# Kernel optimization log

Hardware: AMD Instinct MI355X
Metric: run time of the kernel (lower is better)

Reference implementation:

```python
import jax, jax.numpy as jnp
import numpy as np

NUM_EXPERTS = 8
TOP_K = 2
HIDDEN = 1024
INTER = 3584
BATCH = 2
SEQ = 2048
TOKENS = BATCH * SEQ


def setup_inputs() -> dict:
    key = jax.random.key(0)
    k_h, k_l, k_w1, k_w2, k_w3 = jax.random.split(key, 5)
    hidden_states = jax.random.normal(k_h, (TOKENS, HIDDEN), dtype=jnp.float32)
    # Router: top-2 over softmaxed logits, renormalized (standard Mixtral routing)
    logits = jax.random.normal(k_l, (TOKENS, NUM_EXPERTS), dtype=jnp.float32)
    probs = jax.nn.softmax(logits, axis=-1)
    routing_weights, selected = jax.lax.top_k(probs, TOP_K)  # [T, K], [T, K]
    routing_weights = routing_weights / jnp.sum(routing_weights, axis=-1, keepdims=True)
    # expert_mask: [num_experts, top_k, tokens]
    expert_mask = jax.nn.one_hot(selected, NUM_EXPERTS, dtype=jnp.int32).transpose(2, 1, 0)
    scale = 0.02
    w1 = jax.random.normal(k_w1, (NUM_EXPERTS, HIDDEN, INTER), dtype=jnp.float32) * scale
    w2 = jax.random.normal(k_w2, (NUM_EXPERTS, INTER, HIDDEN), dtype=jnp.float32) * scale
    w3 = jax.random.normal(k_w3, (NUM_EXPERTS, HIDDEN, INTER), dtype=jnp.float32) * scale
    return {
        "expert_mask": expert_mask,
        "hidden_states": hidden_states,
        "routing_weights": routing_weights,
        "w1": w1,
        "w2": w2,
        "w3": w3,
        "batch_size": BATCH,
        "sequence_length": SEQ,
        "hidden_dim": HIDDEN,
    }


def reference(expert_mask, hidden_states, routing_weights, w1, w2, w3,
              batch_size, sequence_length, hidden_dim):
    num_experts = w1.shape[0]
    tokens = batch_size * sequence_length
    # Extra row at the end absorbs writes from fill_value=-1 padding (as in source).
    final = jnp.zeros((tokens + 1, hidden_dim), dtype=hidden_states.dtype)
    for e in range(num_experts):
        # idx: which top-k slot; top_x: which token. Padded with -1.
        idx, top_x = jnp.nonzero(expert_mask[e], size=sequence_length, fill_value=-1)
        cur = hidden_states[top_x]  # [S, H]
        h = (jax.nn.silu(cur @ w1[e]) * (cur @ w3[e])) @ w2[e]  # SwiGLU MLP
        h = h * routing_weights[top_x, idx, None]
        final = final.at[top_x].set(h + final[top_x])
    final = final[:-1]
    return final.reshape(batch_size, sequence_length, hidden_dim)
```

## Files before the change

kernel.cpp:

```cpp
#include <hip/hip_runtime.h>
#include <hip/hip_bf16.h>
#include <cstdint>
#include <cstddef>

#define NEXP  8
#define NTOK  4096
#define HID   1024
#define INTER 3584
#define CAP   2048

#define BM  128
#define BN  128
#define BK  32

typedef __attribute__((ext_vector_type(4))) float floatx4;
typedef __attribute__((ext_vector_type(8))) short shortx8;
typedef unsigned short u16;

__device__ __forceinline__ u16 f2bf(float f) {
    union { float f; unsigned u; } v; v.f = f;
    unsigned r = v.u + 0x7fffu + ((v.u >> 16) & 1u);
    return (u16)(r >> 16);
}

__device__ __forceinline__ shortx8 pack8(const float* v) {
    shortx8 r;
#pragma unroll
    for (int i = 0; i < 8; ++i) r[i] = (short)f2bf(v[i]);
    return r;
}

__device__ __forceinline__ unsigned cvt_pk_bf16(float a, float b) {
    unsigned r;
    asm("v_cvt_pk_bf16_f32 %0, %1, %2" : "=v"(r) : "v"(a), "v"(b));
    return r;
}

__device__ __forceinline__ void async_ld16(const void* g, void* l) {
    __builtin_amdgcn_global_load_lds(
        (const __attribute__((address_space(1))) unsigned int*)g,
        (__attribute__((address_space(3))) unsigned int*)l, 16, 0, 0);
}

__global__ void route_kernel(const int* __restrict__ mask, const float* __restrict__ rw,
                             int* __restrict__ cnt, int* __restrict__ list,
                             float* __restrict__ wgt) {
    int t = blockIdx.x * blockDim.x + threadIdx.x;
    if (t >= NTOK) return;
#pragma unroll
    for (int e = 0; e < NEXP; ++e) {
#pragma unroll
        for (int k = 0; k < 2; ++k) {
            if (mask[(e * 2 + k) * NTOK + t] != 0) {
                int pos = atomicAdd(&cnt[e], 1);
                if (pos < CAP) {
                    list[e * CAP + pos] = t;
                    wgt[e * CAP + pos] = rw[t * 2 + k];
                }
            }
        }
    }
}

__global__ void xcvt_kernel(const float* __restrict__ X, u16* __restrict__ Xb) {
    const int i = (blockIdx.x * 256 + threadIdx.x) * 8;
    float4 a = *(const float4*)&X[i];
    float4 b = *(const float4*)&X[i + 4];
    float v[8] = {a.x, a.y, a.z, a.w, b.x, b.y, b.z, b.w};
    *(shortx8*)&Xb[i] = pack8(v);
}

__global__ void transpose_cvt_kernel(const float* __restrict__ src, u16* __restrict__ dst,
                                     int K, int N) {
    const int e = blockIdx.z;
    src += (size_t)e * K * N;
    dst += (size_t)e * K * N;
    const int n0 = blockIdx.x * 64;
    const int k0 = blockIdx.y * 64;
    __shared__ unsigned ldsT[64 * 34];
    const int tid = threadIdx.x;

    {
        const int np = tid & 15;
        const int kp = tid >> 4;
        const float* sp = src + (size_t)(k0 + kp * 4) * N + n0 + np * 4;
        float4 r0 = *(const float4*)sp;
        float4 r1 = *(const float4*)(sp + (size_t)N);
        float4 r2 = *(const float4*)(sp + 2 * (size_t)N);
        float4 r3 = *(const float4*)(sp + 3 * (size_t)N);
        const float c0[4] = {r0.x, r0.y, r0.z, r0.w};
        const float c1[4] = {r1.x, r1.y, r1.z, r1.w};
        const float c2[4] = {r2.x, r2.y, r2.z, r2.w};
        const float c3[4] = {r3.x, r3.y, r3.z, r3.w};
#pragma unroll
        for (int j = 0; j < 4; ++j) {
            const int n = np * 4 + j;
            uint2 w;
            w.x = cvt_pk_bf16(c0[j], c1[j]);
            w.y = cvt_pk_bf16(c2[j], c3[j]);
            *(uint2*)&ldsT[n * 34 + kp * 2] = w;
        }
    }
    __syncthreads();
    {
        const int n = tid >> 2;
        const int q = tid & 3;
        unsigned r[8];
#pragma unroll
        for (int i = 0; i < 4; ++i) {
            uint2 v = *(const uint2*)&ldsT[n * 34 + (q * 4 + i) * 2];
            r[i * 2] = v.x; r[i * 2 + 1] = v.y;
        }
        u16* dp = dst + (size_t)(n0 + n) * K + k0 + q * 16;
        *(uint4*)&dp[0] = *(const uint4*)&r[0];
        *(uint4*)&dp[8] = *(const uint4*)&r[4];
    }
}

__global__ __launch_bounds__(256, 2)
void gemm1_kernel(const u16* __restrict__ Xb, const u16* __restrict__ W1b,
                  const u16* __restrict__ W3b, const int* __restrict__ cnt,
                  const int* __restrict__ list, const float* __restrict__ wgt,
                  u16* __restrict__ H) {
    const int e  = blockIdx.z;
    const int ce = min(cnt[e], CAP);
    const int m0 = blockIdx.y * BM;
    if (m0 >= ce) return;
    const int n0 = blockIdx.x * BN;

    __shared__ u16 lA [BM * BK];
    __shared__ u16 lB1[BN * BK];
    __shared__ u16 lB3[BN * BK];

    const int tid  = threadIdx.x;
    const int lane = tid & 63;
    const int wave = tid >> 6;

    const int srow0 = wave * 32 + (lane >> 2);
    const int srow1 = srow0 + 16;
    const int scol  = (lane & 3) * 8;
    const int lo0 = wave * 1024 + lane * 8;
    const int lo1 = lo0 + 512;

    const int t0 = list[e * CAP + min(m0 + srow0, ce - 1)];
    const int t1 = list[e * CAP + min(m0 + srow1, ce - 1)];
    const u16* ap0  = Xb + (size_t)t0 * HID + scol;
    const u16* ap1  = Xb + (size_t)t1 * HID + scol;
    const u16* b1p0 = W1b + ((size_t)e * INTER + n0 + srow0) * HID + scol;
    const u16* b1p1 = b1p0 + (size_t)16 * HID;
    const u16* b3p0 = W3b + ((size_t)e * INTER + n0 + srow0) * HID + scol;
    const u16* b3p1 = b3p0 + (size_t)16 * HID;

    const int fl = lane & 15, fq = lane >> 4;
    const int wm  = (wave >> 1) * 64;
    const int wnn = (wave & 1) * 64;

    floatx4 acc1[4][4], acc3[4][4];
#pragma unroll
    for (int i = 0; i < 4; ++i)
#pragma unroll
        for (int j = 0; j < 4; ++j)
#pragma unroll
            for (int r = 0; r < 4; ++r) { acc1[i][j][r] = 0.f; acc3[i][j][r] = 0.f; }

    for (int k0 = 0; k0 < HID; k0 += BK) {
        __syncthreads();
        async_ld16(ap0  + k0, &lA [lo0]);
        async_ld16(ap1  + k0, &lA [lo1]);
        async_ld16(b1p0 + k0, &lB1[lo0]);
        async_ld16(b1p1 + k0, &lB1[lo1]);
        async_ld16(b3p0 + k0, &lB3[lo0]);
        async_ld16(b3p1 + k0, &lB3[lo1]);
        __syncthreads();

        shortx8 af[4], b1f[4], b3f[4];
#pragma unroll
        for (int i = 0; i < 4; ++i)
            af[i] = *(const shortx8*)&lA[(wm + i * 16 + fl) * BK + fq * 8];
#pragma unroll
        for (int j = 0; j < 4; ++j) {
            b1f[j] = *(const shortx8*)&lB1[(wnn + j * 16 + fl) * BK + fq * 8];
            b3f[j] = *(const shortx8*)&lB3[(wnn + j * 16 + fl) * BK + fq * 8];
        }
#pragma unroll
        for (int i = 0; i < 4; ++i)
#pragma unroll
            for (int j = 0; j < 4; ++j) {
                acc1[i][j] = __builtin_amdgcn_mfma_f32_16x16x32_bf16(af[i], b1f[j], acc1[i][j], 0, 0, 0);
                acc3[i][j] = __builtin_amdgcn_mfma_f32_16x16x32_bf16(af[i], b3f[j], acc3[i][j], 0, 0, 0);
            }
    }

#pragma unroll
    for (int i = 0; i < 4; ++i) {
        const int rowb = m0 + wm + i * 16 + fq * 4;
#pragma unroll
        for (int r = 0; r < 4; ++r) {
            const int row = rowb + r;
            const bool valid = row < ce;
            const float rwv = valid ? wgt[e * CAP + row] : 0.f;
            u16* hp = H + (size_t)(e * CAP + (valid ? row : 0)) * INTER;
#pragma unroll
            for (int j = 0; j < 4; ++j) {
                const int col = n0 + wnn + j * 16 + fl;
                float h1 = acc1[i][j][r];
                float h3 = acc3[i][j][r];
                float sv = h1 / (1.f + __expf(-h1)) * h3 * rwv;
                if (valid) hp[col] = f2bf(sv);
            }
        }
    }
}

__global__ __launch_bounds__(256, 2)
void gemm2_kernel(const u16* __restrict__ H, const u16* __restrict__ W2b,
                  const int* __restrict__ cnt, const int* __restrict__ list,
                  float* __restrict__ out) {
    const int e  = blockIdx.z;
    const int ce = min(cnt[e], CAP);
    const int m0 = blockIdx.y * BM;
    if (m0 >= ce) return;
    const int n0 = blockIdx.x * BN;

    __shared__ u16 lA[BM * BK];
    __shared__ u16 lB[BN * BK];

    const int tid  = threadIdx.x;
    const int lane = tid & 63;
    const int wave = tid >> 6;

    const int srow0 = wave * 32 + (lane >> 2);
    const int srow1 = srow0 + 16;
    const int scol  = (lane & 3) * 8;
    const int lo0 = wave * 1024 + lane * 8;
    const int lo1 = lo0 + 512;

    const u16* ap0 = H + (size_t)(e * CAP + m0 + srow0) * INTER + scol;
    const u16* ap1 = ap0 + (size_t)16 * INTER;
    const u16* bp0 = W2b + ((size_t)e * HID + n0 + srow0) * INTER + scol;
    const u16* bp1 = bp0 + (size_t)16 * INTER;

    const int fl = lane & 15, fq = lane >> 4;
    const int wm  = (wave >> 1) * 64;
    const int wnn = (wave & 1) * 64;

    floatx4 acc[4][4];
#pragma unroll
    for (int i = 0; i < 4; ++i)
#pragma unroll
        for (int j = 0; j < 4; ++j)
#pragma unroll
            for (int r = 0; r < 4; ++r) acc[i][j][r] = 0.f;

    for (int k0 = 0; k0 < INTER; k0 += BK) {
        __syncthreads();
        async_ld16(ap0 + k0, &lA[lo0]);
        async_ld16(ap1 + k0, &lA[lo1]);
        async_ld16(bp0 + k0, &lB[lo0]);
        async_ld16(bp1 + k0, &lB[lo1]);
        __syncthreads();

        shortx8 af[4], bf[4];
#pragma unroll
        for (int i = 0; i < 4; ++i)
            af[i] = *(const shortx8*)&lA[(wm + i * 16 + fl) * BK + fq * 8];
#pragma unroll
        for (int j = 0; j < 4; ++j)
            bf[j] = *(const shortx8*)&lB[(wnn + j * 16 + fl) * BK + fq * 8];
#pragma unroll
        for (int i = 0; i < 4; ++i)
#pragma unroll
            for (int j = 0; j < 4; ++j)
                acc[i][j] = __builtin_amdgcn_mfma_f32_16x16x32_bf16(af[i], bf[j], acc[i][j], 0, 0, 0);
    }

#pragma unroll
    for (int i = 0; i < 4; ++i) {
        const int rowb = m0 + wm + i * 16 + fq * 4;
#pragma unroll
        for (int r = 0; r < 4; ++r) {
            const int row = rowb + r;
            const bool valid = row < ce;
            const int tok = valid ? list[e * CAP + row] : 0;
            float* op = out + (size_t)tok * HID;
#pragma unroll
            for (int j = 0; j < 4; ++j) {
                const int col = n0 + wnn + j * 16 + fl;
                if (valid) atomicAdd(&op[col], acc[i][j][r]);
            }
        }
    }
}

extern "C" void kernel_launch(void* const* d_in, const int* in_sizes, int n_in,
                              void* d_out, int out_size, void* d_ws, size_t ws_size,
                              hipStream_t stream) {
    const int*   mask = (const int*)  d_in[0];
    const float* X    = (const float*)d_in[1];
    const float* rw   = (const float*)d_in[2];
    const float* w1   = (const float*)d_in[3];
    const float* w2   = (const float*)d_in[4];
    const float* w3   = (const float*)d_in[5];
    float* out = (float*)d_out;

    char* ws = (char*)d_ws;
    size_t off = 0;
    int*   cnt  = (int*)(ws + off);  off += 256;
    int*   list = (int*)(ws + off);  off += (size_t)NEXP * CAP * 4;
    float* wgt  = (float*)(ws + off); off += (size_t)NEXP * CAP * 4;
    u16*   Xb   = (u16*)(ws + off);  off += (size_t)NTOK * HID * 2;
    u16*   W1b  = (u16*)(ws + off);  off += (size_t)NEXP * HID * INTER * 2;
    u16*   W3b  = (u16*)(ws + off);  off += (size_t)NEXP * HID * INTER * 2;
    u16*   W2b  = (u16*)(ws + off);  off += (size_t)NEXP * HID * INTER * 2;
    u16*   H    = (u16*)(ws + off);  off += (size_t)NEXP * CAP * INTER * 2;

    hipMemsetAsync(cnt, 0, 256, stream);
    hipMemsetAsync(d_out, 0, (size_t)out_size * sizeof(float), stream);

    route_kernel<<<dim3((NTOK + 255) / 256), dim3(256), 0, stream>>>(mask, rw, cnt, list, wgt);
    xcvt_kernel<<<dim3(NTOK * HID / (256 * 8)), dim3(256), 0, stream>>>(X, Xb);
    transpose_cvt_kernel<<<dim3(INTER / 64, HID / 64, NEXP), dim3(256), 0, stream>>>(w1, W1b, HID, INTER);
    transpose_cvt_kernel<<<dim3(INTER / 64, HID / 64, NEXP), dim3(256), 0, stream>>>(w3, W3b, HID, INTER);
    transpose_cvt_kernel<<<dim3(HID / 64, INTER / 64, NEXP), dim3(256), 0, stream>>>(w2, W2b, INTER, HID);

    gemm1_kernel<<<dim3(INTER / BN, CAP / BM, NEXP), dim3(256), 0, stream>>>(Xb, W1b, W3b, cnt, list, wgt, H);
    gemm2_kernel<<<dim3(HID / BN, CAP / BM, NEXP), dim3(256), 0, stream>>>(H, W2b, cnt, list, out);
}
```

Before: 717.8 us.

## Double-buffer LDS in MoE GEMMs with XOR swizzle and merge weight transposes

Both expert GEMM kernels now use a two-stage LDS ring. The next K-tile's async global-to-LDS loads are issued before the current tile's MFMAs, with a single vmcnt wait and barrier per iteration, so load latency overlaps compute. LDS columns are XOR-swizzled on both the store side and the fragment-read side to reduce bank conflicts. The three weight transpose/convert launches are merged into one launch selected by blockIdx.z. LDS use doubles, which could affect the two-blocks-per-CU occupancy target. The swizzle also has to match exactly on both sides to stay correct.

After: 694.1 us. 3.3% less time.

```diff
diff --git a/kernel.cpp b/kernel.cpp
--- a/kernel.cpp
+++ b/kernel.cpp
@@ -40,6 +40,12 @@
     __builtin_amdgcn_global_load_lds(
         (const __attribute__((address_space(1))) unsigned int*)g,
         (__attribute__((address_space(3))) unsigned int*)l, 16, 0, 0);
+}
+
+__device__ __forceinline__ void wait_vm0_barrier() {
+    asm volatile("s_waitcnt vmcnt(0)" ::: "memory");
+    __builtin_amdgcn_s_barrier();
+    __builtin_amdgcn_sched_barrier(0);
 }
 
 __global__ void route_kernel(const int* __restrict__ mask, const float* __restrict__ rw,
@@ -70,16 +76,25 @@
     *(shortx8*)&Xb[i] = pack8(v);
 }
 
-__global__ void transpose_cvt_kernel(const float* __restrict__ src, u16* __restrict__ dst,
-                                     int K, int N) {
-    const int e = blockIdx.z;
+__global__ void transpose_cvt_all_kernel(const float* __restrict__ w1,
+                                         const float* __restrict__ w2,
+                                         const float* __restrict__ w3,
+                                         u16* __restrict__ W1b, u16* __restrict__ W2b,
+                                         u16* __restrict__ W3b) {
+    const int wsel = blockIdx.z;
+    const int e    = blockIdx.y;
+    const float* src; u16* dst; int K, N, nx;
+    if (wsel == 0)      { src = w1; dst = W1b; K = HID;   N = INTER; nx = INTER / 64; }
+    else if (wsel == 1) { src = w3; dst = W3b; K = HID;   N = INTER; nx = INTER / 64; }
+    else                { src = w2; dst = W2b; K = INTER; N = HID;   nx = HID / 64;   }
     src += (size_t)e * K * N;
     dst += (size_t)e * K * N;
-    const int n0 = blockIdx.x * 64;
-    const int k0 = blockIdx.y * 64;
+    const int tile = blockIdx.x;
+    const int n0 = (tile % nx) * 64;
+    const int k0 = (tile / nx) * 64;
+
     __shared__ unsigned ldsT[64 * 34];
     const int tid = threadIdx.x;
-
     {
         const int np = tid & 15;
         const int kp = tid >> 4;
@@ -128,9 +143,7 @@
     if (m0 >= ce) return;
     const int n0 = blockIdx.x * BN;
 
-    __shared__ u16 lA [BM * BK];
-    __shared__ u16 lB1[BN * BK];
-    __shared__ u16 lB3[BN * BK];
+    __shared__ u16 sm[2 * 3 * BM * BK];
 
     const int tid  = threadIdx.x;
     const int lane = tid & 63;
@@ -138,7 +151,8 @@
 
     const int srow0 = wave * 32 + (lane >> 2);
     const int srow1 = srow0 + 16;
-    const int scol  = (lane & 3) * 8;
+    const int s0   = (srow0 >> 1) & 3;
+    const int scol = ((lane & 3) ^ s0) * 8;
     const int lo0 = wave * 1024 + lane * 8;
     const int lo1 = lo0 + 512;
 
@@ -152,9 +166,20 @@
     const u16* b3p1 = b3p0 + (size_t)16 * HID;
 
     const int fl = lane & 15, fq = lane >> 4;
+    const int fqs = (fq ^ ((fl >> 1) & 3)) * 8;
     const int wm  = (wave >> 1) * 64;
     const int wnn = (wave & 1) * 64;
 
+    auto stage = [&](int b, int kk) {
+        u16* base = sm + b * (3 * BM * BK);
+        async_ld16(ap0  + kk, base + lo0);
+        async_ld16(ap1  + kk, base + lo1);
+        async_ld16(b1p0 + kk, base + BM * BK + lo0);
+        async_ld16(b1p1 + kk, base + BM * BK + lo1);
+        async_ld16(b3p0 + kk, base + 2 * BM * BK + lo0);
+        async_ld16(b3p1 + kk, base + 2 * BM * BK + lo1);
+    };
+
     floatx4 acc1[4][4], acc3[4][4];
 #pragma unroll
     for (int i = 0; i < 4; ++i)
@@ -163,24 +188,26 @@
 #pragma unroll
             for (int r = 0; r < 4; ++r) { acc1[i][j][r] = 0.f; acc3[i][j][r] = 0.f; }
 
-    for (int k0 = 0; k0 < HID; k0 += BK) {
-        __syncthreads();
-        async_ld16(ap0  + k0, &lA [lo0]);
-        async_ld16(ap1  + k0, &lA [lo1]);
-        async_ld16(b1p0 + k0, &lB1[lo0]);
-        async_ld16(b1p1 + k0, &lB1[lo1]);
-        async_ld16(b3p0 + k0, &lB3[lo0]);
-        async_ld16(b3p1 + k0, &lB3[lo1]);
-        __syncthreads();
+    const int NT = HID / BK;
+    stage(0, 0);
+    wait_vm0_barrier();
+
+    int cur = 0;
+    for (int t = 0; t < NT; ++t) {
+        if (t + 1 < NT) stage(cur ^ 1, (t + 1) * BK);
+
+        const u16* bA  = sm + cur * (3 * BM * BK);
+        const u16* bB1 = bA + BM * BK;
+        const u16* bB3 = bA + 2 * BM * BK;
 
         shortx8 af[4], b1f[4], b3f[4];
 #pragma unroll
         for (int i = 0; i < 4; ++i)
-            af[i] = *(const shortx8*)&lA[(wm + i * 16 + fl) * BK + fq * 8];
+            af[i] = *(const shortx8*)&bA[(wm + i * 16 + fl) * BK + fqs];
 #pragma unroll
         for (int j = 0; j < 4; ++j) {
-            b1f[j] = *(const shortx8*)&lB1[(wnn + j * 16 + fl) * BK + fq * 8];
-            b3f[j] = *(const shortx8*)&lB3[(wnn + j * 16 + fl) * BK + fq * 8];
+            b1f[j] = *(const shortx8*)&bB1[(wnn + j * 16 + fl) * BK + fqs];
+            b3f[j] = *(const shortx8*)&bB3[(wnn + j * 16 + fl) * BK + fqs];
         }
 #pragma unroll
         for (int i = 0; i < 4; ++i)
@@ -189,6 +216,9 @@
                 acc1[i][j] = __builtin_amdgcn_mfma_f32_16x16x32_bf16(af[i], b1f[j], acc1[i][j], 0, 0, 0);
                 acc3[i][j] = __builtin_amdgcn_mfma_f32_16x16x32_bf16(af[i], b3f[j], acc3[i][j], 0, 0, 0);
             }
+
+        wait_vm0_barrier();
+        cur ^= 1;
     }
 
 #pragma unroll
@@ -222,16 +252,15 @@
     if (m0 >= ce) return;
     const int n0 = blockIdx.x * BN;
 
-    __shared__ u16 lA[BM * BK];
-    __shared__ u16 lB[BN * BK];
+    __shared__ u16 sm[2 * 2 * BM * BK];
 
     const int tid  = threadIdx.x;
     const int lane = tid & 63;
     const int wave = tid >> 6;
 
     const int srow0 = wave * 32 + (lane >> 2);
-    const int srow1 = srow0 + 16;
-    const int scol  = (lane & 3) * 8;
+    const int s0   = (srow0 >> 1) & 3;
+    const int scol = ((lane & 3) ^ s0) * 8;
     const int lo0 = wave * 1024 + lane * 8;
     const int lo1 = lo0 + 512;
 
@@ -241,9 +270,18 @@
     const u16* bp1 = bp0 + (size_t)16 * INTER;
 
     const int fl = lane & 15, fq = lane >> 4;
+    const int fqs = (fq ^ ((fl >> 1) & 3)) * 8;
     const int wm  = (wave >> 1) * 64;
     const int wnn = (wave & 1) * 64;
 
+    auto stage = [&](int b, int kk) {
+        u16* base = sm + b * (2 * BM * BK);
+        async_ld16(ap0 + kk, base + lo0);
+        async_ld16(ap1 + kk, base + lo1);
+        async_ld16(bp0 + kk, base + BM * BK + lo0);
+        async_ld16(bp1 + kk, base + BM * BK + lo1);
+    };
+
     floatx4 acc[4][4];
 #pragma unroll
     for (int i = 0; i < 4; ++i)
@@ -252,26 +290,32 @@
 #pragma unroll
             for (int r = 0; r < 4; ++r) acc[i][j][r] = 0.f;
 
-    for (int k0 = 0; k0 < INTER; k0 += BK) {
-        __syncthreads();
-        async_ld16(ap0 + k0, &lA[lo0]);
-        async_ld16(ap1 + k0, &lA[lo1]);
-        async_ld16(bp0 + k0, &lB[lo0]);
-        async_ld16(bp1 + k0, &lB[lo1]);
-        __syncthreads();
+    const int NT = INTER / BK;
+    stage(0, 0);
+    wait_vm0_barrier();
+
+    int cur = 0;
+    for (int t = 0; t < NT; ++t) {
+        if (t + 1 < NT) stage(cur ^ 1, (t + 1) * BK);
+
+        const u16* bA = sm + cur * (2 * BM * BK);
+        const u16* bB = bA + BM * BK;
 
         shortx8 af[4], bf[4];
 #pragma unroll
         for (int i = 0; i < 4; ++i)
-            af[i] = *(const shortx8*)&lA[(wm + i * 16 + fl) * BK + fq * 8];
+            af[i] = *(const shortx8*)&bA[(wm + i * 16 + fl) * BK + fqs];
 #pragma unroll
         for (int j = 0; j < 4; ++j)
-            bf[j] = *(const shortx8*)&lB[(wnn + j * 16 + fl) * BK + fq * 8];
+            bf[j] = *(const shortx8*)&bB[(wnn + j * 16 + fl) * BK + fqs];
 #pragma unroll
         for (int i = 0; i < 4; ++i)
 #pragma unroll
             for (int j = 0; j < 4; ++j)
                 acc[i][j] = __builtin_amdgcn_mfma_f32_16x16x32_bf16(af[i], bf[j], acc[i][j], 0, 0, 0);
+
+        wait_vm0_barrier();
+        cur ^= 1;
     }
 
 #pragma unroll
@@ -319,9 +363,8 @@
 
     route_kernel<<<dim3((NTOK + 255) / 256), dim3(256), 0, stream>>>(mask, rw, cnt, list, wgt);
     xcvt_kernel<<<dim3(NTOK * HID / (256 * 8)), dim3(256), 0, stream>>>(X, Xb);
-    transpose_cvt_kernel<<<dim3(INTER / 64, HID / 64, NEXP), dim3(256), 0, stream>>>(w1, W1b, HID, INTER);
-    transpose_cvt_kernel<<<dim3(INTER / 64, HID / 64, NEXP), dim3(256), 0, stream>>>(w3, W3b, HID, INTER);
-    transpose_cvt_kernel<<<dim3(HID / 64, INTER / 64, NEXP), dim3(256), 0, stream>>>(w2, W2b, INTER, HID);
+    transpose_cvt_all_kernel<<<dim3((HID / 64) * (INTER / 64), NEXP, 3), dim3(256), 0, stream>>>(
+        w1, w2, w3, W1b, W2b, W3b);
 
     gemm1_kernel<<<dim3(INTER / BN, CAP / BM, NEXP), dim3(256), 0, stream>>>(Xb, W1b, W3b, cnt, list, wgt, H);
     gemm2_kernel<<<dim3(HID / BN, CAP / BM, NEXP), dim3(256), 0, stream>>>(H, W2b, cnt, list, out);
```
